# Kernel optimization log

Measured on AMD Instinct MI355X. Metric: run time of the kernel, lower is better.

The kernel has to match this reference:

```python
import jax, jax.numpy as jnp
import numpy as np

B, H, S, DK, DV = 2, 16, 2048, 64, 64

def setup_inputs() -> dict:
    key = jax.random.key(0)
    k1, k2, k3 = jax.random.split(key, 3)
    Q = jax.random.normal(k1, (B, H, S, DK), dtype=jnp.float32)
    K = jax.random.normal(k2, (B, H, S, DK), dtype=jnp.float32)
    V = jax.random.normal(k3, (B, H, S, DV), dtype=jnp.float32)
    mask = jnp.zeros((1, 1, S, S), dtype=jnp.float32)  # additive mask, broadcastable
    return {"Q": Q, "K": K, "V": V, "mask": mask}

def reference(Q, K, V, mask):
    d_k = Q.shape[-1]
    scale = 1.0 / jnp.sqrt(jnp.asarray(d_k, dtype=Q.dtype))
    # [..., q, k] = Q @ K^T / sqrt(d_k) + mask (additive)
    logits = jnp.einsum('bhqd,bhkd->bhqk', Q, K) * scale + mask
    attn = jax.nn.softmax(logits, axis=-1)
    return jnp.einsum('bhqk,bhkv->bhqv', attn, V)
```

## Files before the change

### kernel.cpp

```cpp
#include <hip/hip_runtime.h>
#include <hip/hip_bf16.h>


constexpr int Bn = 2, Hn = 16, Sn = 2048, DKn = 64;
constexpr int WAVES = 4, QSUB = 2;
constexpr int QB = WAVES * QSUB * 16;
constexpr int KVB = 64;
constexpr int NIT = Sn / KVB;
constexpr float SCALE = 0.125f;

typedef __attribute__((ext_vector_type(8))) short bf16x8;
typedef __attribute__((ext_vector_type(4))) short bf16x4;
typedef __attribute__((ext_vector_type(4))) float f32x4;

union Frag { bf16x8 v; unsigned short s[8]; };
union H4   { bf16x4 v; unsigned short s[4]; };

__device__ __forceinline__ unsigned short f2bf(float x) {
  union { float f; unsigned u; } c; c.f = x;
  unsigned r = c.u + 0x7FFFu + ((c.u >> 16) & 1u);
  return (unsigned short)(r >> 16);
}

__global__ __launch_bounds__(256, 2) void sdpa_fa2(
    const float* __restrict__ Q, const float* __restrict__ K,
    const float* __restrict__ V, const float* __restrict__ M,
    float* __restrict__ Out) {
  __shared__ unsigned short Kt[64 * 64];
  __shared__ unsigned short Vt[64 * 64];
  __shared__ unsigned short Pt[WAVES * 16 * 64];

  const int tid = threadIdx.x;
  const int lane = tid & 63;
  const int wave = tid >> 6;
  const int q16 = lane & 15;
  const int h4 = lane >> 4;

  int bid = blockIdx.x;
  bid = (bid & 7) * ((int)gridDim.x >> 3) + (bid >> 3);
  const int head = bid / (Sn / QB);
  const int qblk = bid % (Sn / QB);
  const int q0w = qblk * QB + wave * (QSUB * 16);

  const float* __restrict__ Qh = Q + (size_t)head * Sn * DKn;
  const float* __restrict__ Kh = K + (size_t)head * Sn * DKn;
  const float* __restrict__ Vh = V + (size_t)head * Sn * DKn;
  float* __restrict__ Oh = Out + (size_t)head * Sn * DKn;

  Frag qf[QSUB][2];
#pragma unroll
  for (int s = 0; s < QSUB; ++s)
#pragma unroll
    for (int kc = 0; kc < 2; ++kc) {
      const float* p = Qh + (size_t)(q0w + s * 16 + q16) * DKn + kc * 32 + h4 * 8;
#pragma unroll
      for (int j = 0; j < 8; ++j) qf[s][kc].s[j] = f2bf(p[j]);
    }

  f32x4 acc[QSUB][4];
  float m_run[QSUB], l_run[QSUB];
#pragma unroll
  for (int s = 0; s < QSUB; ++s) {
    m_run[s] = -1e30f; l_run[s] = 0.f;
#pragma unroll
    for (int dt = 0; dt < 4; ++dt) acc[s][dt] = (f32x4){0.f, 0.f, 0.f, 0.f};
  }

  const int krow = tid >> 2, kcb = tid & 3;
  const int vk4 = tid >> 4, vcb = tid & 15;

  f32x4 kr[4], vr[4];
  {
    const float* kp = Kh + (size_t)krow * DKn + kcb * 16;
#pragma unroll
    for (int u = 0; u < 4; ++u) kr[u] = *(const f32x4*)(kp + 4 * u);
    const float* vp = Vh + (size_t)(4 * vk4) * DKn + vcb * 4;
#pragma unroll
    for (int r = 0; r < 4; ++r) vr[r] = *(const f32x4*)(vp + (size_t)r * DKn);
  }

  for (int it = 0; it < NIT; ++it) {
    const int kv0 = it * KVB;
    __syncthreads();

#pragma unroll
    for (int b = 0; b < 2; ++b) {
      Frag fr;
#pragma unroll
      for (int j = 0; j < 8; ++j) fr.s[j] = f2bf(kr[2 * b + (j >> 2)][j & 3]);
      const int c16p = (2 * kcb + b) ^ (krow & 7);
      *(bf16x8*)&Kt[krow * 64 + c16p * 8] = fr.v;
    }
#pragma unroll
    for (int j = 0; j < 4; ++j) {
      H4 ph;
#pragma unroll
      for (int r = 0; r < 4; ++r) ph.s[r] = f2bf(vr[r][j]);
      const int d = 4 * vcb + j;
      const int c16p = (vk4 >> 1) ^ (d & 7);
      *(bf16x4*)&Vt[d * 64 + c16p * 8 + (vk4 & 1) * 4] = ph.v;
    }
    __syncthreads();

    if (it + 1 < NIT) {
      const float* kp = Kh + (size_t)(kv0 + KVB + krow) * DKn + kcb * 16;
#pragma unroll
      for (int u = 0; u < 4; ++u) kr[u] = *(const f32x4*)(kp + 4 * u);
      const float* vp = Vh + (size_t)(kv0 + KVB + 4 * vk4) * DKn + vcb * 4;
#pragma unroll
      for (int r = 0; r < 4; ++r) vr[r] = *(const f32x4*)(vp + (size_t)r * DKn);
    }

    Frag kf[4][2], vf[4][2];
#pragma unroll
    for (int t = 0; t < 4; ++t)
#pragma unroll
      for (int kc = 0; kc < 2; ++kc)
        kf[t][kc].v = *(const bf16x8*)&Kt[(16 * t + q16) * 64 + ((4 * kc + h4) ^ (q16 & 7)) * 8];
#pragma unroll
    for (int dt = 0; dt < 4; ++dt)
#pragma unroll
      for (int c = 0; c < 2; ++c)
        vf[dt][c].v = *(const bf16x8*)&Vt[(dt * 16 + q16) * 64 + ((4 * c + h4) ^ (q16 & 7)) * 8];

#pragma unroll
    for (int s = 0; s < QSUB; ++s) {
      const int q = q0w + s * 16 + q16;
      const float* mrow = M + (size_t)q * Sn + kv0;
      f32x4 mk[4];
#pragma unroll
      for (int t = 0; t < 4; ++t) mk[t] = *(const f32x4*)(mrow + 16 * t + 4 * h4);

      f32x4 st[4];
      __builtin_amdgcn_s_setprio(1);
#pragma unroll
      for (int t = 0; t < 4; ++t) {
        f32x4 z = (f32x4){0.f, 0.f, 0.f, 0.f};
        z = __builtin_amdgcn_mfma_f32_16x16x32_bf16(kf[t][0].v, qf[s][0].v, z, 0, 0, 0);
        st[t] = __builtin_amdgcn_mfma_f32_16x16x32_bf16(kf[t][1].v, qf[s][1].v, z, 0, 0, 0);
      }
      __builtin_amdgcn_s_setprio(0);

      float sv[4][4];
      float mx = -1e30f;
#pragma unroll
      for (int t = 0; t < 4; ++t)
#pragma unroll
        for (int r = 0; r < 4; ++r) {
          sv[t][r] = st[t][r] * SCALE + mk[t][r];
          mx = fmaxf(mx, sv[t][r]);
        }
      mx = fmaxf(mx, __shfl_xor(mx, 16, 64));
      mx = fmaxf(mx, __shfl_xor(mx, 32, 64));

      const float mn = fmaxf(m_run[s], mx);
      const float corr = __expf(m_run[s] - mn);
      m_run[s] = mn;

      float ps = 0.f;
#pragma unroll
      for (int t = 0; t < 4; ++t) {
        H4 ph;
#pragma unroll
        for (int r = 0; r < 4; ++r) {
          const float p = __expf(sv[t][r] - mn);
          ps += p;
          ph.s[r] = f2bf(p);
        }
        *(bf16x4*)&Pt[wave * 1024 + q16 * 64 + ((2 * t + (h4 >> 1)) ^ (q16 & 7)) * 8 + (h4 & 1) * 4] = ph.v;
      }
      ps += __shfl_xor(ps, 16, 64);
      ps += __shfl_xor(ps, 32, 64);
      l_run[s] = l_run[s] * corr + ps;

#pragma unroll
      for (int dt = 0; dt < 4; ++dt)
#pragma unroll
        for (int r = 0; r < 4; ++r) acc[s][dt][r] *= corr;

      Frag pf[2];
#pragma unroll
      for (int c = 0; c < 2; ++c)
        pf[c].v = *(const bf16x8*)&Pt[wave * 1024 + q16 * 64 + ((4 * c + h4) ^ (q16 & 7)) * 8];

      __builtin_amdgcn_s_setprio(1);
#pragma unroll
      for (int dt = 0; dt < 4; ++dt)
#pragma unroll
        for (int c = 0; c < 2; ++c)
          acc[s][dt] = __builtin_amdgcn_mfma_f32_16x16x32_bf16(vf[dt][c].v, pf[c].v, acc[s][dt], 0, 0, 0);
      __builtin_amdgcn_s_setprio(0);
    }
  }

#pragma unroll
  for (int s = 0; s < QSUB; ++s) {
    const float inv = 1.0f / l_run[s];
    const int q = q0w + s * 16 + q16;
#pragma unroll
    for (int dt = 0; dt < 4; ++dt) {
      f32x4 o = acc[s][dt];
      o[0] *= inv; o[1] *= inv; o[2] *= inv; o[3] *= inv;
      *(f32x4*)&Oh[(size_t)q * DKn + dt * 16 + 4 * h4] = o;
    }
  }
}

extern "C" void kernel_launch(void* const* d_in, const int* in_sizes, int n_in,
                              void* d_out, int out_size, void* d_ws, size_t ws_size,
                              hipStream_t stream) {
  const float* Q = (const float*)d_in[0];
  const float* K = (const float*)d_in[1];
  const float* V = (const float*)d_in[2];
  const float* M = (const float*)d_in[3];
  float* O = (float*)d_out;
  dim3 grid(Bn * Hn * (Sn / QB));
  sdpa_fa2<<<grid, dim3(256), 0, stream>>>(Q, K, V, M, O);
}
```

Measured before the change: 205.3 us.

## Rewrite attention kernel with 32x32 MFMA, double-buffered KV, register P, lazy rescale

Result: faster. 190.7 us (-7.1%).

```diff
diff --git a/kernel.cpp b/kernel.cpp
--- a/kernel.cpp
+++ b/kernel.cpp
@@ -1,208 +1,232 @@
 #include <hip/hip_runtime.h>
-#include <hip/hip_bf16.h>
-
-
-constexpr int Bn = 2, Hn = 16, Sn = 2048, DKn = 64;
-constexpr int WAVES = 4, QSUB = 2;
-constexpr int QB = WAVES * QSUB * 16;
+
+
+constexpr int Bn = 2, Hn = 16, Sn = 2048, Dn = 64;
+constexpr int QB = 128;
 constexpr int KVB = 64;
 constexpr int NIT = Sn / KVB;
 constexpr float SCALE = 0.125f;
+constexpr float DEFER_THR = 8.0f;
 
 typedef __attribute__((ext_vector_type(8))) short bf16x8;
-typedef __attribute__((ext_vector_type(4))) short bf16x4;
 typedef __attribute__((ext_vector_type(4))) float f32x4;
-
-union Frag { bf16x8 v; unsigned short s[8]; };
-union H4   { bf16x4 v; unsigned short s[4]; };
-
-__device__ __forceinline__ unsigned short f2bf(float x) {
-  union { float f; unsigned u; } c; c.f = x;
-  unsigned r = c.u + 0x7FFFu + ((c.u >> 16) & 1u);
-  return (unsigned short)(r >> 16);
+typedef __attribute__((ext_vector_type(16))) float f32x16;
+
+union FragU { bf16x8 v; unsigned u[4]; };
+
+__device__ __forceinline__ unsigned cvt_pk(float lo, float hi) {
+  unsigned r;
+  asm("v_cvt_pk_bf16_f32 %0, %1, %2" : "=v"(r) : "v"(lo), "v"(hi));
+  return r;
 }
 
-__global__ __launch_bounds__(256, 2) void sdpa_fa2(
+__global__ __launch_bounds__(256, 2) void sdpa_fa3(
     const float* __restrict__ Q, const float* __restrict__ K,
     const float* __restrict__ V, const float* __restrict__ M,
     float* __restrict__ Out) {
-  __shared__ unsigned short Kt[64 * 64];
-  __shared__ unsigned short Vt[64 * 64];
-  __shared__ unsigned short Pt[WAVES * 16 * 64];
+  __shared__ unsigned short Kt[2][64 * 64];
+  __shared__ unsigned short Vt[2][64 * 64];
 
   const int tid = threadIdx.x;
   const int lane = tid & 63;
   const int wave = tid >> 6;
-  const int q16 = lane & 15;
-  const int h4 = lane >> 4;
+  const int l31 = lane & 31;
+  const int hi = lane >> 5;
+  const int l7 = lane & 7;
 
   int bid = blockIdx.x;
   bid = (bid & 7) * ((int)gridDim.x >> 3) + (bid >> 3);
-  const int head = bid / (Sn / QB);
-  const int qblk = bid % (Sn / QB);
-  const int q0w = qblk * QB + wave * (QSUB * 16);
-
-  const float* __restrict__ Qh = Q + (size_t)head * Sn * DKn;
-  const float* __restrict__ Kh = K + (size_t)head * Sn * DKn;
-  const float* __restrict__ Vh = V + (size_t)head * Sn * DKn;
-  float* __restrict__ Oh = Out + (size_t)head * Sn * DKn;
-
-  Frag qf[QSUB][2];
-#pragma unroll
-  for (int s = 0; s < QSUB; ++s)
-#pragma unroll
-    for (int kc = 0; kc < 2; ++kc) {
-      const float* p = Qh + (size_t)(q0w + s * 16 + q16) * DKn + kc * 32 + h4 * 8;
-#pragma unroll
-      for (int j = 0; j < 8; ++j) qf[s][kc].s[j] = f2bf(p[j]);
-    }
-
-  f32x4 acc[QSUB][4];
-  float m_run[QSUB], l_run[QSUB];
-#pragma unroll
-  for (int s = 0; s < QSUB; ++s) {
-    m_run[s] = -1e30f; l_run[s] = 0.f;
-#pragma unroll
-    for (int dt = 0; dt < 4; ++dt) acc[s][dt] = (f32x4){0.f, 0.f, 0.f, 0.f};
-  }
+  const int head = bid >> 4;
+  const int qblk = bid & 15;
+  const int qrow = qblk * QB + wave * 32 + l31;
+
+  const float* __restrict__ Qh = Q + (size_t)head * Sn * Dn;
+  const float* __restrict__ Kh = K + (size_t)head * Sn * Dn;
+  const float* __restrict__ Vh = V + (size_t)head * Sn * Dn;
+  float* __restrict__ Oh = Out + (size_t)head * Sn * Dn;
+  const float* __restrict__ Mrow = M + (size_t)qrow * Sn;
+
+  FragU qf[4];
+#pragma unroll
+  for (int kc = 0; kc < 4; ++kc) {
+    const float* p = Qh + (size_t)qrow * Dn + kc * 16 + hi * 8;
+    f32x4 a = *(const f32x4*)p;
+    f32x4 b = *(const f32x4*)(p + 4);
+    qf[kc].u[0] = cvt_pk(a[0] * SCALE, a[1] * SCALE);
+    qf[kc].u[1] = cvt_pk(a[2] * SCALE, a[3] * SCALE);
+    qf[kc].u[2] = cvt_pk(b[0] * SCALE, b[1] * SCALE);
+    qf[kc].u[3] = cvt_pk(b[2] * SCALE, b[3] * SCALE);
+  }
+
+  f32x16 acc0, acc1;
+#pragma unroll
+  for (int i = 0; i < 16; ++i) { acc0[i] = 0.f; acc1[i] = 0.f; }
+  float m_run = -1e30f, l_run = 0.f;
 
   const int krow = tid >> 2, kcb = tid & 3;
   const int vk4 = tid >> 4, vcb = tid & 15;
 
   f32x4 kr[4], vr[4];
   {
-    const float* kp = Kh + (size_t)krow * DKn + kcb * 16;
+    const float* kp = Kh + (size_t)krow * Dn + kcb * 16;
 #pragma unroll
     for (int u = 0; u < 4; ++u) kr[u] = *(const f32x4*)(kp + 4 * u);
-    const float* vp = Vh + (size_t)(4 * vk4) * DKn + vcb * 4;
-#pragma unroll
-    for (int r = 0; r < 4; ++r) vr[r] = *(const f32x4*)(vp + (size_t)r * DKn);
-  }
+    const float* vp = Vh + (size_t)(4 * vk4) * Dn + vcb * 4;
+#pragma unroll
+    for (int r = 0; r < 4; ++r) vr[r] = *(const f32x4*)(vp + (size_t)r * Dn);
+#pragma unroll
+    for (int b = 0; b < 2; ++b) {
+      FragU f;
+      f.u[0] = cvt_pk(kr[2 * b][0], kr[2 * b][1]);
+      f.u[1] = cvt_pk(kr[2 * b][2], kr[2 * b][3]);
+      f.u[2] = cvt_pk(kr[2 * b + 1][0], kr[2 * b + 1][1]);
+      f.u[3] = cvt_pk(kr[2 * b + 1][2], kr[2 * b + 1][3]);
+      const int pos = (2 * kcb + b) ^ (krow & 7);
+      *(bf16x8*)&Kt[0][krow * 64 + pos * 8] = f.v;
+    }
+#pragma unroll
+    for (int j = 0; j < 4; ++j) {
+      const int d = 4 * vcb + j;
+      unsigned w0 = cvt_pk(vr[0][j], vr[1][j]);
+      unsigned w1 = cvt_pk(vr[2][j], vr[3][j]);
+      const int pos = (vk4 >> 1) ^ (d & 7);
+      unsigned* dst = (unsigned*)&Vt[0][d * 64 + pos * 8 + (vk4 & 1) * 4];
+      dst[0] = w0; dst[1] = w1;
+    }
+  }
+  __syncthreads();
 
   for (int it = 0; it < NIT; ++it) {
     const int kv0 = it * KVB;
+    const int cur = it & 1;
+    const unsigned short* Kb = Kt[cur];
+    const unsigned short* Vb = Vt[cur];
+
+    if (it + 1 < NIT) {
+      const float* kp = Kh + (size_t)(kv0 + KVB + krow) * Dn + kcb * 16;
+#pragma unroll
+      for (int u = 0; u < 4; ++u) kr[u] = *(const f32x4*)(kp + 4 * u);
+      const float* vp = Vh + (size_t)(kv0 + KVB + 4 * vk4) * Dn + vcb * 4;
+#pragma unroll
+      for (int r = 0; r < 4; ++r) vr[r] = *(const f32x4*)(vp + (size_t)r * Dn);
+    }
+
+#pragma unroll
+    for (int t = 0; t < 2; ++t) {
+      f32x4 mk[4];
+#pragma unroll
+      for (int m = 0; m < 4; ++m)
+        mk[m] = *(const f32x4*)(Mrow + kv0 + 32 * t + 8 * m + 4 * hi);
+
+      f32x16 st;
+#pragma unroll
+      for (int i = 0; i < 16; ++i) st[i] = 0.f;
+      __builtin_amdgcn_s_setprio(1);
+#pragma unroll
+      for (int kc = 0; kc < 4; ++kc) {
+        FragU kf;
+        kf.v = *(const bf16x8*)&Kb[(32 * t + l31) * 64 + (((2 * kc + hi) ^ l7) * 8)];
+        st = __builtin_amdgcn_mfma_f32_32x32x16_bf16(kf.v, qf[kc].v, st, 0, 0, 0);
+      }
+      __builtin_amdgcn_s_setprio(0);
+
+      float p[16];
+#pragma unroll
+      for (int m = 0; m < 4; ++m)
+#pragma unroll
+        for (int e = 0; e < 4; ++e) p[4 * m + e] = st[4 * m + e] + mk[m][e];
+
+      float t8[8];
+#pragma unroll
+      for (int i = 0; i < 8; ++i) t8[i] = fmaxf(p[2 * i], p[2 * i + 1]);
+      float t4a = fmaxf(t8[0], t8[1]), t4b = fmaxf(t8[2], t8[3]);
+      float t4c = fmaxf(t8[4], t8[5]), t4d = fmaxf(t8[6], t8[7]);
+      float mx = fmaxf(fmaxf(t4a, t4b), fmaxf(t4c, t4d));
+      mx = fmaxf(mx, __shfl_xor(mx, 32, 64));
+
+      if (!__all(mx <= m_run + DEFER_THR)) {
+        const float mn = fmaxf(m_run, mx);
+        const float corr = __expf(m_run - mn);
+        m_run = mn;
+        l_run *= corr;
+#pragma unroll
+        for (int i = 0; i < 16; ++i) { acc0[i] *= corr; acc1[i] *= corr; }
+      }
+
+      float ps = 0.f;
+#pragma unroll
+      for (int i = 0; i < 16; ++i) {
+        p[i] = __expf(p[i] - m_run);
+        ps += p[i];
+      }
+      ps += __shfl_xor(ps, 32, 64);
+      l_run += ps;
+
+      unsigned W[4][2];
+#pragma unroll
+      for (int m = 0; m < 4; ++m)
+#pragma unroll
+        for (int s = 0; s < 2; ++s)
+          W[m][s] = cvt_pk(p[4 * m + 2 * s], p[4 * m + 2 * s + 1]);
+
+      FragU pf[2];
+#pragma unroll
+      for (int cc = 0; cc < 2; ++cc)
+#pragma unroll
+        for (int s = 0; s < 2; ++s) {
+          const unsigned a = W[2 * cc][s];
+          const unsigned b = W[2 * cc + 1][s];
+          const unsigned pa = (unsigned)__shfl_xor((int)a, 32, 64);
+          const unsigned pb = (unsigned)__shfl_xor((int)b, 32, 64);
+          pf[cc].u[s] = hi ? pb : a;
+          pf[cc].u[2 + s] = hi ? b : pa;
+        }
+
+      __builtin_amdgcn_s_setprio(1);
+#pragma unroll
+      for (int cc = 0; cc < 2; ++cc) {
+        const int c = 2 * t + cc;
+        FragU vf0, vf1;
+        vf0.v = *(const bf16x8*)&Vb[(l31) * 64 + (((2 * c + hi) ^ l7) * 8)];
+        vf1.v = *(const bf16x8*)&Vb[(32 + l31) * 64 + (((2 * c + hi) ^ l7) * 8)];
+        acc0 = __builtin_amdgcn_mfma_f32_32x32x16_bf16(vf0.v, pf[cc].v, acc0, 0, 0, 0);
+        acc1 = __builtin_amdgcn_mfma_f32_32x32x16_bf16(vf1.v, pf[cc].v, acc1, 0, 0, 0);
+      }
+      __builtin_amdgcn_s_setprio(0);
+    }
+
+    if (it + 1 < NIT) {
+#pragma unroll
+      for (int b = 0; b < 2; ++b) {
+        FragU f;
+        f.u[0] = cvt_pk(kr[2 * b][0], kr[2 * b][1]);
+        f.u[1] = cvt_pk(kr[2 * b][2], kr[2 * b][3]);
+        f.u[2] = cvt_pk(kr[2 * b + 1][0], kr[2 * b + 1][1]);
+        f.u[3] = cvt_pk(kr[2 * b + 1][2], kr[2 * b + 1][3]);
+        const int pos = (2 * kcb + b) ^ (krow & 7);
+        *(bf16x8*)&Kt[cur ^ 1][krow * 64 + pos * 8] = f.v;
+      }
+#pragma unroll
+      for (int j = 0; j < 4; ++j) {
+        const int d = 4 * vcb + j;
+        unsigned w0 = cvt_pk(vr[0][j], vr[1][j]);
+        unsigned w1 = cvt_pk(vr[2][j], vr[3][j]);
+        const int pos = (vk4 >> 1) ^ (d & 7);
+        unsigned* dst = (unsigned*)&Vt[cur ^ 1][d * 64 + pos * 8 + (vk4 & 1) * 4];
+        dst[0] = w0; dst[1] = w1;
+      }
+    }
     __syncthreads();
-
-#pragma unroll
-    for (int b = 0; b < 2; ++b) {
-      Frag fr;
-#pragma unroll
-      for (int j = 0; j < 8; ++j) fr.s[j] = f2bf(kr[2 * b + (j >> 2)][j & 3]);
-      const int c16p = (2 * kcb + b) ^ (krow & 7);
-      *(bf16x8*)&Kt[krow * 64 + c16p * 8] = fr.v;
-    }
-#pragma unroll
-    for (int j = 0; j < 4; ++j) {
-      H4 ph;
-#pragma unroll
-      for (int r = 0; r < 4; ++r) ph.s[r] = f2bf(vr[r][j]);
-      const int d = 4 * vcb + j;
-      const int c16p = (vk4 >> 1) ^ (d & 7);
-      *(bf16x4*)&Vt[d * 64 + c16p * 8 + (vk4 & 1) * 4] = ph.v;
-    }
-    __syncthreads();
-
-    if (it + 1 < NIT) {
-      const float* kp = Kh + (size_t)(kv0 + KVB + krow) * DKn + kcb * 16;
-#pragma unroll
-      for (int u = 0; u < 4; ++u) kr[u] = *(const f32x4*)(kp + 4 * u);
-      const float* vp = Vh + (size_t)(kv0 + KVB + 4 * vk4) * DKn + vcb * 4;
-#pragma unroll
-      for (int r = 0; r < 4; ++r) vr[r] = *(const f32x4*)(vp + (size_t)r * DKn);
-    }
-
-    Frag kf[4][2], vf[4][2];
-#pragma unroll
-    for (int t = 0; t < 4; ++t)
-#pragma unroll
-      for (int kc = 0; kc < 2; ++kc)
-        kf[t][kc].v = *(const bf16x8*)&Kt[(16 * t + q16) * 64 + ((4 * kc + h4) ^ (q16 & 7)) * 8];
-#pragma unroll
-    for (int dt = 0; dt < 4; ++dt)
-#pragma unroll
-      for (int c = 0; c < 2; ++c)
-        vf[dt][c].v = *(const bf16x8*)&Vt[(dt * 16 + q16) * 64 + ((4 * c + h4) ^ (q16 & 7)) * 8];
-
-#pragma unroll
-    for (int s = 0; s < QSUB; ++s) {
-      const int q = q0w + s * 16 + q16;
-      const float* mrow = M + (size_t)q * Sn + kv0;
-      f32x4 mk[4];
-#pragma unroll
-      for (int t = 0; t < 4; ++t) mk[t] = *(const f32x4*)(mrow + 16 * t + 4 * h4);
-
-      f32x4 st[4];
-      __builtin_amdgcn_s_setprio(1);
-#pragma unroll
-      for (int t = 0; t < 4; ++t) {
-        f32x4 z = (f32x4){0.f, 0.f, 0.f, 0.f};
-        z = __builtin_amdgcn_mfma_f32_16x16x32_bf16(kf[t][0].v, qf[s][0].v, z, 0, 0, 0);
-        st[t] = __builtin_amdgcn_mfma_f32_16x16x32_bf16(kf[t][1].v, qf[s][1].v, z, 0, 0, 0);
-      }
-      __builtin_amdgcn_s_setprio(0);
-
-      float sv[4][4];
-      float mx = -1e30f;
-#pragma unroll
-      for (int t = 0; t < 4; ++t)
-#pragma unroll
-        for (int r = 0; r < 4; ++r) {
-          sv[t][r] = st[t][r] * SCALE + mk[t][r];
-          mx = fmaxf(mx, sv[t][r]);
-        }
-      mx = fmaxf(mx, __shfl_xor(mx, 16, 64));
-      mx = fmaxf(mx, __shfl_xor(mx, 32, 64));
-
-      const float mn = fmaxf(m_run[s], mx);
-      const float corr = __expf(m_run[s] - mn);
-      m_run[s] = mn;
-
-      float ps = 0.f;
-#pragma unroll
-      for (int t = 0; t < 4; ++t) {
-        H4 ph;
-#pragma unroll
-        for (int r = 0; r < 4; ++r) {
-          const float p = __expf(sv[t][r] - mn);
-          ps += p;
-          ph.s[r] = f2bf(p);
-        }
-        *(bf16x4*)&Pt[wave * 1024 + q16 * 64 + ((2 * t + (h4 >> 1)) ^ (q16 & 7)) * 8 + (h4 & 1) * 4] = ph.v;
-      }
-      ps += __shfl_xor(ps, 16, 64);
-      ps += __shfl_xor(ps, 32, 64);
-      l_run[s] = l_run[s] * corr + ps;
-
-#pragma unroll
-      for (int dt = 0; dt < 4; ++dt)
-#pragma unroll
-        for (int r = 0; r < 4; ++r) acc[s][dt][r] *= corr;
-
-      Frag pf[2];
-#pragma unroll
-      for (int c = 0; c < 2; ++c)
-        pf[c].v = *(const bf16x8*)&Pt[wave * 1024 + q16 * 64 + ((4 * c + h4) ^ (q16 & 7)) * 8];
-
-      __builtin_amdgcn_s_setprio(1);
-#pragma unroll
-      for (int dt = 0; dt < 4; ++dt)
-#pragma unroll
-        for (int c = 0; c < 2; ++c)
-          acc[s][dt] = __builtin_amdgcn_mfma_f32_16x16x32_bf16(vf[dt][c].v, pf[c].v, acc[s][dt], 0, 0, 0);
-      __builtin_amdgcn_s_setprio(0);
-    }
-  }
-
-#pragma unroll
-  for (int s = 0; s < QSUB; ++s) {
-    const float inv = 1.0f / l_run[s];
-    const int q = q0w + s * 16 + q16;
-#pragma unroll
-    for (int dt = 0; dt < 4; ++dt) {
-      f32x4 o = acc[s][dt];
-      o[0] *= inv; o[1] *= inv; o[2] *= inv; o[3] *= inv;
-      *(f32x4*)&Oh[(size_t)q * DKn + dt * 16 + 4 * h4] = o;
-    }
+  }
+
+  const float inv = 1.0f / l_run;
+#pragma unroll
+  for (int m = 0; m < 4; ++m) {
+    f32x4 o0, o1;
+#pragma unroll
+    for (int e = 0; e < 4; ++e) { o0[e] = acc0[4 * m + e] * inv; o1[e] = acc1[4 * m + e] * inv; }
+    *(f32x4*)&Oh[(size_t)qrow * Dn + 8 * m + 4 * hi] = o0;
+    *(f32x4*)&Oh[(size_t)qrow * Dn + 32 + 8 * m + 4 * hi] = o1;
   }
 }
 
@@ -215,5 +239,5 @@
   const float* M = (const float*)d_in[3];
   float* O = (float*)d_out;
   dim3 grid(Bn * Hn * (Sn / QB));
-  sdpa_fa2<<<grid, dim3(256), 0, stream>>>(Q, K, V, M, O);
+  sdpa_fa3<<<grid, dim3(256), 0, stream>>>(Q, K, V, M, O);
 }
```
